# Performance work log

Measured on AMD Instinct MI355X. Metric: run time of the kernel, lower is better.

Reference implementation:

```python
import jax, jax.numpy as jnp
import numpy as np

N = 100000   # nodes
E = 800000   # undirected (unique) edges; directed count = 2*E
DV = 128; DE = 16; DH = 128; DO = 128
G = 64       # graphs in batch


def setup_inputs() -> dict:
    key = jax.random.key(0)
    ks = jax.random.split(key, 8)
    x = jax.random.normal(ks[0], (N, DV), jnp.float32)
    edge_index = jax.random.randint(ks[1], (2, 2 * E), 0, N, dtype=jnp.int32)
    edge_attr = jax.random.normal(ks[2], (E, DE), jnp.float32)
    batch = jnp.sort(jax.random.randint(ks[3], (N,), 0, G, dtype=jnp.int32))
    s = lambda k, shp, fan: jax.random.normal(k, shp, jnp.float32) / np.sqrt(fan)
    W_gcn = s(ks[4], (DV, DH), DV); b_gcn = jnp.zeros((DH,), jnp.float32)
    W_le = s(ks[5], (DE, DH), DE); b_le = jnp.zeros((DH,), jnp.float32)
    W_lin = s(ks[6], (2 * DH, DH), 2 * DH); b_lin = jnp.zeros((DH,), jnp.float32)
    W_out = s(ks[7], (DH, DO), DH); b_out = jnp.zeros((DO,), jnp.float32)
    return dict(x=x, edge_index=edge_index, edge_attr=edge_attr, batch=batch,
                W_gcn=W_gcn, b_gcn=b_gcn, W_le=W_le, b_le=b_le,
                W_lin=W_lin, b_lin=b_lin, W_out=W_out, b_out=b_out)


def reference(x, edge_index, edge_attr, batch,
              W_gcn, b_gcn, W_le, b_le, W_lin, b_lin, W_out, b_out):
    n = x.shape[0]
    loop = jnp.arange(n, dtype=edge_index.dtype)
    src = jnp.concatenate([edge_index[0], loop])  # [2E+N] with self loops
    dst = jnp.concatenate([edge_index[1], loop])

    # ---- GCNConv: symmetric norm, self-loops, lin then aggregate, + bias ----
    xw = x @ W_gcn                                      # [N, DH]
    ones_e = jnp.ones(src.shape[0], jnp.float32)
    deg = jax.ops.segment_sum(ones_e, dst, num_segments=n)  # >=1 via self loops
    dinv = jax.lax.rsqrt(deg)
    norm = dinv[src] * dinv[dst]                        # [2E+N]
    h = jax.ops.segment_sum(norm[:, None] * xw[src], dst, num_segments=n) + b_gcn
    h = jax.nn.relu(h)

    # ---- EdgeGCN: duplicate edge_attr per direction, self-loop attr = ones ----
    ea2 = jnp.repeat(edge_attr, 2, axis=0)              # [2E, DE] interleaved
    ea_full = jnp.concatenate([ea2, jnp.ones((n, edge_attr.shape[1]), jnp.float32)])
    edge_feat = ea_full @ W_le + b_le                   # [2E+N, DH]
    x_j = h[src]                                        # gather source node feats
    msg = jnp.concatenate([x_j, edge_feat], axis=-1) @ W_lin + b_lin
    h2 = jax.ops.segment_sum(msg, dst, num_segments=n)  # aggr='add'
    h2 = jax.nn.relu(h2)

    # ---- global mean pool + final linear ----
    cnt = jax.ops.segment_sum(jnp.ones(n, jnp.float32), batch, num_segments=G)
    pooled = jax.ops.segment_sum(h2, batch, num_segments=G) / jnp.maximum(cnt, 1.0)[:, None]
    return pooled @ W_out + b_out                       # [G, DO]
```

## Files before the change

### kernel.cpp

```cpp
#include <hip/hip_runtime.h>
#include <hip/hip_bf16.h>
#include <cstddef>

typedef unsigned int  u32;
typedef unsigned short u16;
typedef __attribute__((ext_vector_type(8))) short short8;
typedef __attribute__((ext_vector_type(4))) float f32x4;
typedef __attribute__((ext_vector_type(2))) float f32x2;

#define DV 128
#define DH 128
#define DE 16
#define DO 128

__device__ inline float bf_lo(u32 u){ return __uint_as_float(u << 16); }
__device__ inline float bf_hi(u32 u){ return __uint_as_float(u & 0xFFFF0000u); }
__device__ inline u32 fpack2(float a, float b){
  u32 ua = __float_as_uint(a), ub = __float_as_uint(b);
  ua += 0x7FFFu + ((ua >> 16) & 1u);
  ub += 0x7FFFu + ((ub >> 16) & 1u);
  return (ua >> 16) | (ub & 0xFFFF0000u);
}
__device__ inline u16 f2bf(float a){
  u32 ua = __float_as_uint(a); ua += 0x7FFFu + ((ua >> 16) & 1u); return (u16)(ua >> 16);
}

__device__ inline void acc_fp8(u32 s, float& a0, float& a1, float& a2, float& a3){
  f32x2 lo = __builtin_amdgcn_cvt_pk_f32_fp8((int)s, false);
  f32x2 hi = __builtin_amdgcn_cvt_pk_f32_fp8((int)s, true);
  a0 += lo.x; a1 += lo.y; a2 += hi.x; a3 += hi.y;
}
__device__ inline u32 pack_fp8(float a0, float a1, float a2, float a3){
  int o = __builtin_amdgcn_cvt_pk_fp8_f32(a0, a1, 0, false);
  o = __builtin_amdgcn_cvt_pk_fp8_f32(a2, a3, o, true);
  return (u32)o;
}

__global__ void k_init(int* cnt, float* poolp, int2* ce,
                       u32* xws_zrow, u32* h_zrow,
                       int n, int pn, int cefill, int nmark){
  int v = blockIdx.x * blockDim.x + threadIdx.x;
  if (v < n) cnt[v] = 0;
  if (v < pn) poolp[v] = 0.f;
  if (v < cefill) ce[v] = make_int2(nmark, 0);
  if (v < 32){ xws_zrow[v] = 0u; h_zrow[v] = 0u; }
}

__global__ void k_count(const int* dst, const float* edge_attr, int* cnt, int* rank,
                        u32* ea_pack, int e2){
  int j = blockIdx.x * blockDim.x + threadIdx.x;
  if (j < e2){
    rank[j] = atomicAdd(&cnt[dst[j]], 1);
    float4 f0 = *(const float4*)(edge_attr + (size_t)j * 8);
    float4 f1 = *(const float4*)(edge_attr + (size_t)j * 8 + 4);
    uint4 o;
    o.x = fpack2(f0.x, f0.y); o.y = fpack2(f0.z, f0.w);
    o.z = fpack2(f1.x, f1.y); o.w = fpack2(f1.z, f1.w);
    *(uint4*)(ea_pack + (size_t)j * 4) = o;
  }
}

__global__ __launch_bounds__(256) void k_scan1(const int* cnt, int* partial, int* bsums, int n){
  __shared__ int lds[256];
  int t = threadIdx.x;
  int base = blockIdx.x * 1024 + t * 4;
  int v0=0,v1=0,v2=0,v3=0;
  if (base + 3 < n){ int4 q = *(const int4*)(cnt + base); v0=q.x; v1=q.y; v2=q.z; v3=q.w; }
  else {
    if (base + 0 < n) v0 = cnt[base];
    if (base + 1 < n) v1 = cnt[base+1];
    if (base + 2 < n) v2 = cnt[base+2];
  }
  v0 = (v0 + 7) & ~7; v1 = (v1 + 7) & ~7; v2 = (v2 + 7) & ~7; v3 = (v3 + 7) & ~7;
  v1 += v0; v2 += v1; v3 += v2;
  lds[t] = v3; __syncthreads();
  for (int off = 1; off < 256; off <<= 1){
    int x = (t >= off) ? lds[t - off] : 0;
    __syncthreads();
    lds[t] += x;
    __syncthreads();
  }
  int add = (t > 0) ? lds[t - 1] : 0;
  if (base + 3 < n){
    int4 q; q.x = v0+add; q.y = v1+add; q.z = v2+add; q.w = v3+add;
    *(int4*)(partial + base) = q;
  } else {
    if (base + 0 < n) partial[base]   = v0 + add;
    if (base + 1 < n) partial[base+1] = v1 + add;
    if (base + 2 < n) partial[base+2] = v2 + add;
  }
  if (t == 255) bsums[blockIdx.x] = lds[255];
}

__global__ __launch_bounds__(256) void k_scan3w(const int* partial, const int* bsums, int nb,
                                                int* row_ptr, const int* cnt,
                                                float* dinv, float* degf,
                                                const int* batch, int* startg, int n, int g, int NB,
                                                const float* W_lin, const float* b_lin,
                                                const float* W_le, const float* b_le, float* Wfull){
  int bid = blockIdx.x;
  int t = threadIdx.x;
  if (bid >= NB){
    int r = (bid - NB) * 2 + (t >> 7), c = t & 127;
    if (r < DH){
      Wfull[r * DH + c] = W_lin[r * DH + c];
    } else if (r < DH + DE){
      int i = r - DH;
      float acc = 0.f;
      #pragma unroll 8
      for (int k = 0; k < DH; k += 4){
        float4 wl = *(const float4*)(W_le + i * DH + k);
        acc += wl.x * W_lin[(size_t)(DH + k    ) * DH + c];
        acc += wl.y * W_lin[(size_t)(DH + k + 1) * DH + c];
        acc += wl.z * W_lin[(size_t)(DH + k + 2) * DH + c];
        acc += wl.w * W_lin[(size_t)(DH + k + 3) * DH + c];
      }
      Wfull[r * DH + c] = acc;
    } else if (r == 144){
      float acc = b_lin[c];
      #pragma unroll 8
      for (int k = 0; k < DH; k += 4){
        float4 bl = *(const float4*)(b_le + k);
        acc += bl.x * W_lin[(size_t)(DH + k    ) * DH + c];
        acc += bl.y * W_lin[(size_t)(DH + k + 1) * DH + c];
        acc += bl.z * W_lin[(size_t)(DH + k + 2) * DH + c];
        acc += bl.w * W_lin[(size_t)(DH + k + 3) * DH + c];
      }
      Wfull[r * DH + c] = acc;
    } else if (r < 160){
      Wfull[r * DH + c] = 0.f;
    }
    return;
  }
  __shared__ int lds[128];
  if (t < 128) lds[t] = (t < nb) ? bsums[t] : 0;
  __syncthreads();
  for (int off = 1; off < 128; off <<= 1){
    int x = (t >= off && t < 128) ? lds[t - off] : 0;
    __syncthreads();
    if (t < 128) lds[t] += x;
    __syncthreads();
  }
  int i = bid * 256 + t;
  if (i < n){
    int chunk = i >> 10;
    int add = (chunk > 0) ? lds[chunk - 1] : 0;
    row_ptr[i + 1] = partial[i] + add;
    if (i == 0) row_ptr[0] = 0;
    float c = (float)(cnt[i] + 1);
    dinv[i] = rsqrtf(c);
    degf[i] = c;
    int b = batch[i];
    int prev = (i == 0) ? -1 : batch[i - 1];
    for (int q = prev + 1; q <= b; ++q) startg[q] = i;
    if (i == n - 1){ for (int q = b + 1; q <= g; ++q) startg[q] = n; }
  }
}

__global__ void k_scatter(const int* src, const int* dst, const int* rank,
                          const int* row_ptr, int2* ce, int e2){
  int j = blockIdx.x * blockDim.x + threadIdx.x;
  if (j < e2){
    int d = dst[j];
    int pos = row_ptr[d] + rank[j];
    ce[pos] = make_int2(src[j] << 5, j >> 1);
  }
}

template<int K, bool RELU, bool ABF16, bool SCALE, bool OFP8, bool POOL>
__global__ __launch_bounds__(256) void k_gemm_mfma(const void* Ap, const float* W, u32* outb,
                                                   const float* scale, int M,
                                                   const int* batchp, float* poolp){
  constexpr int SA = K + 8;
  constexpr int CS = 136;
  __shared__ u16 Wt[128 * SA];
  __shared__ u16 At[64 * SA];
  int tid = threadIdx.x;
  int row0 = blockIdx.x * 64;

  {
    int c = tid & 127, half = tid >> 7;
    for (int g = half; g < K / 8; g += 2){
      int k0 = g * 8;
      float w0 = W[(size_t)(k0+0)*128 + c], w1 = W[(size_t)(k0+1)*128 + c];
      float w2 = W[(size_t)(k0+2)*128 + c], w3 = W[(size_t)(k0+3)*128 + c];
      float w4 = W[(size_t)(k0+4)*128 + c], w5 = W[(size_t)(k0+5)*128 + c];
      float w6 = W[(size_t)(k0+6)*128 + c], w7 = W[(size_t)(k0+7)*128 + c];
      uint4 pk;
      pk.x = fpack2(w0, w1); pk.y = fpack2(w2, w3);
      pk.z = fpack2(w4, w5); pk.w = fpack2(w6, w7);
      *(uint4*)&Wt[c * SA + k0] = pk;
    }
  }
  constexpr int CH = K / 8;
  for (int idx = tid; idx < 64 * CH; idx += 256){
    int r = idx / CH, ch = idx - r * CH;
    int gr = row0 + r; if (gr > M - 1) gr = M - 1;
    uint4 pk;
    if (ABF16){
      pk = *(const uint4*)((const u16*)Ap + (size_t)gr * K + ch * 8);
    } else {
      const float* A = (const float*)Ap + (size_t)gr * K + ch * 8;
      float4 q0 = *(const float4*)A;
      float4 q1 = *(const float4*)(A + 4);
      pk.x = fpack2(q0.x, q0.y); pk.y = fpack2(q0.z, q0.w);
      pk.z = fpack2(q1.x, q1.y); pk.w = fpack2(q1.z, q1.w);
    }
    *(uint4*)&At[r * SA + ch * 8] = pk;
  }
  __syncthreads();

  int l = tid & 63, w = tid >> 6;
  int m = l & 15, quad = l >> 4;
  f32x4 acc[8];
  #pragma unroll
  for (int ct = 0; ct < 8; ++ct) acc[ct] = (f32x4){0.f, 0.f, 0.f, 0.f};
  #pragma unroll
  for (int ks = 0; ks < K; ks += 32){
    short8 av = *(const short8*)&At[(w * 16 + m) * SA + ks + quad * 8];
    #pragma unroll
    for (int ct = 0; ct < 8; ++ct){
      short8 bv = *(const short8*)&Wt[(ct * 16 + m) * SA + ks + quad * 8];
      acc[ct] = __builtin_amdgcn_mfma_f32_16x16x32_bf16(av, bv, acc[ct], 0, 0, 0);
    }
  }
  __syncthreads();

  if (POOL){
    float* ps = (float*)At;
    int rbase = w * 16 + quad * 4;
    int g0 = batchp[row0];
    int glast = batchp[(row0 + 63 < M) ? (row0 + 63) : (M - 1)];
    if (g0 == glast){
      #pragma unroll
      for (int ct = 0; ct < 8; ++ct){
        float s = 0.f;
        #pragma unroll
        for (int r = 0; r < 4; ++r){
          float vv = fmaxf(acc[ct][r], 0.f);
          if (row0 + rbase + r < M) s += vv;
        }
        s += __shfl_xor(s, 16);
        s += __shfl_xor(s, 32);
        if (quad == 0) ps[w * 128 + ct * 16 + m] = s;
      }
      __syncthreads();
      if (tid < 128){
        float t = ps[tid] + ps[128 + tid] + ps[256 + tid] + ps[384 + tid];
        atomicAdd(&poolp[g0 * DO + tid], t);
      }
    } else {
      #pragma unroll
      for (int ct = 0; ct < 8; ++ct){
        #pragma unroll
        for (int r = 0; r < 4; ++r){
          int row = row0 + rbase + r;
          if (row < M){
            float vv = fmaxf(acc[ct][r], 0.f);
            atomicAdd(&poolp[batchp[row] * DO + ct * 16 + m], vv);
          }
        }
      }
    }
    return;
  }

  u16* Ct = At;
  float sc[4];
  if (SCALE){
    #pragma unroll
    for (int r = 0; r < 4; ++r){
      int gr = row0 + w * 16 + quad * 4 + r;
      sc[r] = scale[gr < M ? gr : (M - 1)];
    }
  }
  #pragma unroll
  for (int ct = 0; ct < 8; ++ct){
    #pragma unroll
    for (int r = 0; r < 4; ++r){
      float vv = acc[ct][r];
      if (SCALE) vv *= sc[r];
      if (RELU)  vv = fmaxf(vv, 0.f);
      Ct[(w * 16 + quad * 4 + r) * CS + ct * 16 + m] = f2bf(vv);
    }
  }
  __syncthreads();
  if (OFP8){
    for (int idx = tid; idx < 64 * 16; idx += 256){
      int r = idx >> 4, c8 = idx & 15;
      int gr = row0 + r;
      if (gr < M){
        uint4 qv = *(const uint4*)&Ct[r * CS + c8 * 8];
        uint2 ov;
        ov.x = (u32)__builtin_amdgcn_cvt_pk_fp8_f32(bf_lo(qv.y), bf_hi(qv.y),
               __builtin_amdgcn_cvt_pk_fp8_f32(bf_lo(qv.x), bf_hi(qv.x), 0, false), true);
        ov.y = (u32)__builtin_amdgcn_cvt_pk_fp8_f32(bf_lo(qv.w), bf_hi(qv.w),
               __builtin_amdgcn_cvt_pk_fp8_f32(bf_lo(qv.z), bf_hi(qv.z), 0, false), true);
        *(uint2*)(outb + (size_t)gr * 32 + c8 * 2) = ov;
      }
    }
  } else {
    for (int idx = tid; idx < 64 * 16; idx += 256){
      int r = idx >> 4, ch = idx & 15;
      int gr = row0 + r;
      if (gr < M){
        uint4 q = *(const uint4*)&Ct[r * CS + ch * 8];
        *(uint4*)(outb + (size_t)gr * 64 + ch * 4) = q;
      }
    }
  }
}

__global__ __launch_bounds__(256) void k_phase1(const u32* xws8, const int* row_ptr, const int2* ce,
                                                const float* dinv, const float* b_gcn, u32* h8, int n){
  int lane = threadIdx.x & 63;
  int ln = lane & 31;
  int v = blockIdx.x * 8 + ((threadIdx.x >> 6) << 1) + (lane >> 5);
  if (v >= n) return;
  u32 sp = xws8[(size_t)v * 32 + ln];
  float a0 = 0.f, a1 = 0.f, a2 = 0.f, a3 = 0.f;
  acc_fp8(sp, a0, a1, a2, a3);
  int e0 = row_ptr[v], e1 = row_ptr[v + 1];
  int i = e0;
  u32 q0=0,q1=0,q2=0,q3=0,q4=0,q5=0,q6=0,q7=0;
  if (i < e1){
    const int4* cp = (const int4*)(ce + i);
    int4 A = cp[0], B = cp[1], C = cp[2], D = cp[3];
    q0 = xws8[A.x + ln]; q1 = xws8[A.z + ln];
    q2 = xws8[B.x + ln]; q3 = xws8[B.z + ln];
    q4 = xws8[C.x + ln]; q5 = xws8[C.z + ln];
    q6 = xws8[D.x + ln]; q7 = xws8[D.z + ln];
  }
  for (; i + 8 < e1; i += 8){
    const int4* cp2 = (const int4*)(ce + i + 8);
    int4 A = cp2[0], B = cp2[1], C = cp2[2], D = cp2[3];
    u32 p0 = xws8[A.x + ln], p1 = xws8[A.z + ln];
    u32 p2 = xws8[B.x + ln], p3 = xws8[B.z + ln];
    u32 p4 = xws8[C.x + ln], p5 = xws8[C.z + ln];
    u32 p6 = xws8[D.x + ln], p7 = xws8[D.z + ln];
    acc_fp8(q0, a0, a1, a2, a3); acc_fp8(q1, a0, a1, a2, a3);
    acc_fp8(q2, a0, a1, a2, a3); acc_fp8(q3, a0, a1, a2, a3);
    acc_fp8(q4, a0, a1, a2, a3); acc_fp8(q5, a0, a1, a2, a3);
    acc_fp8(q6, a0, a1, a2, a3); acc_fp8(q7, a0, a1, a2, a3);
    q0=p0; q1=p1; q2=p2; q3=p3; q4=p4; q5=p5; q6=p6; q7=p7;
  }
  if (i < e1){
    acc_fp8(q0, a0, a1, a2, a3); acc_fp8(q1, a0, a1, a2, a3);
    acc_fp8(q2, a0, a1, a2, a3); acc_fp8(q3, a0, a1, a2, a3);
    acc_fp8(q4, a0, a1, a2, a3); acc_fp8(q5, a0, a1, a2, a3);
    acc_fp8(q6, a0, a1, a2, a3); acc_fp8(q7, a0, a1, a2, a3);
  }
  float dv = dinv[v];
  float4 bg = *(const float4*)(b_gcn + ln * 4);
  a0 = fmaxf(fmaf(dv, a0, bg.x), 0.f);
  a1 = fmaxf(fmaf(dv, a1, bg.y), 0.f);
  a2 = fmaxf(fmaf(dv, a2, bg.z), 0.f);
  a3 = fmaxf(fmaf(dv, a3, bg.w), 0.f);
  h8[(size_t)v * 32 + ln] = pack_fp8(a0, a1, a2, a3);
}

__global__ __launch_bounds__(256) void k_phase2(const u32* h8, const int* row_ptr, const int2* ce,
                                                const u16* ea_bf, const float* degf,
                                                u16* A2b, int n){
  int lane = threadIdx.x & 63;
  int ln = lane & 31;
  int half = lane >> 5;
  int v = blockIdx.x * 8 + ((threadIdx.x >> 6) << 1) + half;
  if (v >= n) return;
  u32 sp = h8[(size_t)v * 32 + ln];
  float a0 = 0.f, a1 = 0.f, a2 = 0.f, a3 = 0.f;
  acc_fp8(sp, a0, a1, a2, a3);
  float es = 0.f;
  int ch = ln & 15, grp = ln >> 4;
  int nmark = n << 5;
  int e0 = row_ptr[v], e1 = row_ptr[v + 1];
  int i = e0;
  u32 q0=0,q1=0,q2=0,q3=0,q4=0,q5=0,q6=0,q7=0;
  int4 A = {0,0,0,0}, B = {0,0,0,0}, C = {0,0,0,0}, D = {0,0,0,0};
  if (i < e1){
    const int4* cp = (const int4*)(ce + i);
    A = cp[0]; B = cp[1]; C = cp[2]; D = cp[3];
    q0 = h8[A.x + ln]; q1 = h8[A.z + ln];
    q2 = h8[B.x + ln]; q3 = h8[B.z + ln];
    q4 = h8[C.x + ln]; q5 = h8[C.z + ln];
    q6 = h8[D.x + ln]; q7 = h8[D.z + ln];
  }
  for (; i + 8 < e1; i += 8){
    const int4* cp2 = (const int4*)(ce + i + 8);
    int4 A2 = cp2[0], B2 = cp2[1], C2 = cp2[2], D2 = cp2[3];
    int s0x = grp ? C.x : A.x, s0e = grp ? C.y : A.y;
    int s1x = grp ? C.z : A.z, s1e = grp ? C.w : A.w;
    int s2x = grp ? D.x : B.x, s2e = grp ? D.y : B.y;
    int s3x = grp ? D.z : B.z, s3e = grp ? D.w : B.w;
    float v0 = bf_lo((u32)ea_bf[(size_t)s0e * 16 + ch]);
    float v1 = bf_lo((u32)ea_bf[(size_t)s1e * 16 + ch]);
    float v2 = bf_lo((u32)ea_bf[(size_t)s2e * 16 + ch]);
    float v3 = bf_lo((u32)ea_bf[(size_t)s3e * 16 + ch]);
    u32 p0 = h8[A2.x + ln], p1 = h8[A2.z + ln];
    u32 p2 = h8[B2.x + ln], p3 = h8[B2.z + ln];
    u32 p4 = h8[C2.x + ln], p5 = h8[C2.z + ln];
    u32 p6 = h8[D2.x + ln], p7 = h8[D2.z + ln];
    acc_fp8(q0, a0, a1, a2, a3); acc_fp8(q1, a0, a1, a2, a3);
    acc_fp8(q2, a0, a1, a2, a3); acc_fp8(q3, a0, a1, a2, a3);
    acc_fp8(q4, a0, a1, a2, a3); acc_fp8(q5, a0, a1, a2, a3);
    acc_fp8(q6, a0, a1, a2, a3); acc_fp8(q7, a0, a1, a2, a3);
    es = fmaf((s0x != nmark) ? 1.f : 0.f, v0, es);
    es = fmaf((s1x != nmark) ? 1.f : 0.f, v1, es);
    es = fmaf((s2x != nmark) ? 1.f : 0.f, v2, es);
    es = fmaf((s3x != nmark) ? 1.f : 0.f, v3, es);
    q0=p0; q1=p1; q2=p2; q3=p3; q4=p4; q5=p5; q6=p6; q7=p7;
    A=A2; B=B2; C=C2; D=D2;
  }
  if (i < e1){
    int s0x = grp ? C.x : A.x, s0e = grp ? C.y : A.y;
    int s1x = grp ? C.z : A.z, s1e = grp ? C.w : A.w;
    int s2x = grp ? D.x : B.x, s2e = grp ? D.y : B.y;
    int s3x = grp ? D.z : B.z, s3e = grp ? D.w : B.w;
    float v0 = bf_lo((u32)ea_bf[(size_t)s0e * 16 + ch]);
    float v1 = bf_lo((u32)ea_bf[(size_t)s1e * 16 + ch]);
    float v2 = bf_lo((u32)ea_bf[(size_t)s2e * 16 + ch]);
    float v3 = bf_lo((u32)ea_bf[(size_t)s3e * 16 + ch]);
    acc_fp8(q0, a0, a1, a2, a3); acc_fp8(q1, a0, a1, a2, a3);
    acc_fp8(q2, a0, a1, a2, a3); acc_fp8(q3, a0, a1, a2, a3);
    acc_fp8(q4, a0, a1, a2, a3); acc_fp8(q5, a0, a1, a2, a3);
    acc_fp8(q6, a0, a1, a2, a3); acc_fp8(q7, a0, a1, a2, a3);
    es = fmaf((s0x != nmark) ? 1.f : 0.f, v0, es);
    es = fmaf((s1x != nmark) ? 1.f : 0.f, v1, es);
    es = fmaf((s2x != nmark) ? 1.f : 0.f, v2, es);
    es = fmaf((s3x != nmark) ? 1.f : 0.f, v3, es);
  }
  es += __shfl_xor(es, 16);
  float c0v = __shfl(es, half * 32 + (ln & 7) * 2);
  float c1v = __shfl(es, half * 32 + (ln & 7) * 2 + 1);
  u32* rowp = (u32*)(A2b + (size_t)v * 160);
  uint2 o; o.x = fpack2(a0, a1); o.y = fpack2(a2, a3);
  *(uint2*)(rowp + ln * 2) = o;
  if (ln < 8){
    rowp[64 + ln] = fpack2(c0v + 1.0f, c1v + 1.0f);
  } else if (ln < 16){
    rowp[64 + ln] = (ln == 8) ? (u32)f2bf(degf[v]) : 0u;
  }
}

__global__ __launch_bounds__(128) void k_poolb_final(const float* poolp, const int* start,
                                                     const float* W_out, const float* b_out,
                                                     float* out){
  __shared__ float pl[DH];
  int g = blockIdx.x, c = threadIdx.x;
  int cntg = start[g + 1] - start[g]; if (cntg < 1) cntg = 1;
  pl[c] = poolp[g * DO + c] / (float)cntg;
  __syncthreads();
  float acc = b_out[c];
  for (int k = 0; k < DH; ++k) acc += pl[k] * W_out[k * DO + c];
  out[g * DO + c] = acc;
}

extern "C" void kernel_launch(void* const* d_in, const int* in_sizes, int n_in,
                              void* d_out, int out_size, void* d_ws, size_t ws_size,
                              hipStream_t stream){
  const float* x         = (const float*)d_in[0];
  const int*   edge_index= (const int*)  d_in[1];
  const float* edge_attr = (const float*)d_in[2];
  const int*   batch     = (const int*)  d_in[3];
  const float* W_gcn     = (const float*)d_in[4];
  const float* b_gcn     = (const float*)d_in[5];
  const float* W_le      = (const float*)d_in[6];
  const float* b_le      = (const float*)d_in[7];
  const float* W_lin     = (const float*)d_in[8];
  const float* b_lin     = (const float*)d_in[9];
  const float* W_out     = (const float*)d_in[10];
  const float* b_out     = (const float*)d_in[11];
  float* out = (float*)d_out;

  const int n  = in_sizes[0] / DV;
  const int e2 = in_sizes[1] / 2;
  const int g  = out_size / DO;
  const int* srcp = edge_index;
  const int* dstp = edge_index + e2;
  const int e2pad = e2 + 7 * n + 8;

  char* ws = (char*)d_ws;
  size_t off = 0;
  auto alloc = [&](size_t bytes) -> char* {
    char* p = ws + off; off = (off + bytes + 255) & ~(size_t)255; return p;
  };

  int*   cnt     = (int*)  alloc((size_t)n * 4);
  int*   row_ptr = (int*)  alloc((size_t)(n + 1) * 4);
  int*   rank    = (int*)  alloc((size_t)e2 * 4);
  int*   partial = (int*)  alloc((size_t)n * 4);
  int*   bsums   = (int*)  alloc(512);
  float* dinv    = (float*)alloc((size_t)n * 4);
  float* degf    = (float*)alloc((size_t)n * 4);
  int*   startg  = (int*)  alloc((size_t)(g + 1) * 4);
  float* poolp   = (float*)alloc((size_t)g * DO * 4);
  float* Wfull   = (float*)alloc(160 * DH * 4);
  u32*   h8      = (u32*)  alloc((size_t)(n + 1) * 128);
  int2*  ce      = (int2*) alloc((size_t)e2pad * 8);
  u32*   ea_bf   = (u32*)  alloc((size_t)e2 * 16);
  size_t szXW = (size_t)(n + 1) * 128, szA2 = (size_t)n * 160 * 2;
  char* regionA = alloc(szA2 > szXW ? szA2 : szXW);
  u32* xws8 = (u32*)regionA;
  u16* A2b  = (u16*)regionA;

  const int nb1024 = (n + 1023) / 1024;
  const int NB = (n + 255) / 256;

  k_init   <<<(e2pad + 255) / 256, 256, 0, stream>>>(cnt, poolp, ce,
                                                     xws8 + (size_t)n * 32, h8 + (size_t)n * 32,
                                                     n, g * DO, e2pad, n << 5);
  k_count  <<<(e2 + 255) / 256, 256, 0, stream>>>(dstp, edge_attr, cnt, rank, ea_bf, e2);
  k_scan1  <<<nb1024, 256, 0, stream>>>(cnt, partial, bsums, n);
  k_scan3w <<<NB + 80, 256, 0, stream>>>(partial, bsums, nb1024, row_ptr, cnt, dinv, degf,
                                         batch, startg, n, g, NB,
                                         W_lin, b_lin, W_le, b_le, Wfull);
  k_scatter<<<(e2 + 255) / 256, 256, 0, stream>>>(srcp, dstp, rank, row_ptr, ce, e2);

  k_gemm_mfma<DV, false, false, true, true, false>
      <<<(n + 63) / 64, 256, 0, stream>>>(x, W_gcn, xws8, dinv, n, nullptr, nullptr);
  k_phase1 <<<(n + 7) / 8, 256, 0, stream>>>(xws8, row_ptr, ce, dinv, b_gcn, h8, n);
  k_phase2 <<<(n + 7) / 8, 256, 0, stream>>>(h8, row_ptr, ce,
                                             (const u16*)ea_bf, degf, A2b, n);
  k_gemm_mfma<160, true, true, false, false, true>
      <<<(n + 63) / 64, 256, 0, stream>>>(A2b, Wfull, (u32*)nullptr, (const float*)nullptr,
                                          n, batch, poolp);
  k_poolb_final<<<g, 128, 0, stream>>>(poolp, startg, W_out, b_out, out);
}
```

Before: 421.9 us.

## Merge edge scatter with first GEMM in one launch; move ce padding fill into count

```diff
diff --git a/kernel.cpp b/kernel.cpp
--- a/kernel.cpp
+++ b/kernel.cpp
@@ -36,19 +36,17 @@
   return (u32)o;
 }
 
-__global__ void k_init(int* cnt, float* poolp, int2* ce,
-                       u32* xws_zrow, u32* h_zrow,
-                       int n, int pn, int cefill, int nmark){
+__global__ void k_init(int* cnt, float* poolp, u32* xws_zrow, u32* h_zrow, int n, int pn){
   int v = blockIdx.x * blockDim.x + threadIdx.x;
   if (v < n) cnt[v] = 0;
   if (v < pn) poolp[v] = 0.f;
-  if (v < cefill) ce[v] = make_int2(nmark, 0);
   if (v < 32){ xws_zrow[v] = 0u; h_zrow[v] = 0u; }
 }
 
 __global__ void k_count(const int* dst, const float* edge_attr, int* cnt, int* rank,
-                        u32* ea_pack, int e2){
+                        u32* ea_pack, int2* ce, int e2, int cefill, int nmark){
   int j = blockIdx.x * blockDim.x + threadIdx.x;
+  int tot = gridDim.x * blockDim.x;
   if (j < e2){
     rank[j] = atomicAdd(&cnt[dst[j]], 1);
     float4 f0 = *(const float4*)(edge_attr + (size_t)j * 8);
@@ -58,6 +56,8 @@
     o.z = fpack2(f1.x, f1.y); o.w = fpack2(f1.z, f1.w);
     *(uint4*)(ea_pack + (size_t)j * 4) = o;
   }
+  int2 pd = make_int2(nmark, 0);
+  for (int i = j; i < cefill; i += tot) ce[i] = pd;
 }
 
 __global__ __launch_bounds__(256) void k_scan1(const int* cnt, int* partial, int* bsums, int n){
@@ -157,13 +157,94 @@
   }
 }
 
-__global__ void k_scatter(const int* src, const int* dst, const int* rank,
-                          const int* row_ptr, int2* ce, int e2){
-  int j = blockIdx.x * blockDim.x + threadIdx.x;
-  if (j < e2){
-    int d = dst[j];
-    int pos = row_ptr[d] + rank[j];
-    ce[pos] = make_int2(src[j] << 5, j >> 1);
+__global__ __launch_bounds__(256) void k_scatter_g1(const int* src, const int* dst, const int* rank,
+                                                    const int* row_ptr, int2* ce, int e2, int SB,
+                                                    const float* x, const float* W,
+                                                    const float* dinv, u32* xws8, int M){
+  __shared__ u16 lds_u[64 * 136];
+  int bid = blockIdx.x;
+  int tid = threadIdx.x;
+  if (bid < SB){
+    int j = bid * 256 + tid;
+    if (j < e2){
+      int d = dst[j];
+      int pos = row_ptr[d] + rank[j];
+      ce[pos] = make_int2(src[j] << 5, j >> 1);
+    }
+    return;
+  }
+  int row0 = (bid - SB) * 64;
+  u16* Wt = lds_u;
+  u16* At = lds_u + 128 * 40;
+  int l = tid & 63, w = tid >> 6;
+  int m = l & 15, quad = l >> 4;
+  f32x4 acc[8];
+  #pragma unroll
+  for (int ct = 0; ct < 8; ++ct) acc[ct] = (f32x4){0.f, 0.f, 0.f, 0.f};
+  for (int ks = 0; ks < DV; ks += 32){
+    __syncthreads();
+    {
+      int c = tid & 127, hh = tid >> 7;
+      #pragma unroll
+      for (int g2 = 0; g2 < 2; ++g2){
+        int k0 = hh * 16 + g2 * 8;
+        const float* Wp = W + (size_t)(ks + k0) * 128 + c;
+        float w0 = Wp[0*128], w1 = Wp[1*128], w2 = Wp[2*128], w3 = Wp[3*128];
+        float w4 = Wp[4*128], w5 = Wp[5*128], w6 = Wp[6*128], w7 = Wp[7*128];
+        uint4 pk;
+        pk.x = fpack2(w0, w1); pk.y = fpack2(w2, w3);
+        pk.z = fpack2(w4, w5); pk.w = fpack2(w6, w7);
+        *(uint4*)&Wt[c * 40 + k0] = pk;
+      }
+    }
+    {
+      int r = tid >> 2, ch = tid & 3;
+      int gr = row0 + r; if (gr > M - 1) gr = M - 1;
+      const float* A = x + (size_t)gr * DV + ks + ch * 8;
+      float4 q0 = *(const float4*)A;
+      float4 q1 = *(const float4*)(A + 4);
+      uint4 pk;
+      pk.x = fpack2(q0.x, q0.y); pk.y = fpack2(q0.z, q0.w);
+      pk.z = fpack2(q1.x, q1.y); pk.w = fpack2(q1.z, q1.w);
+      *(uint4*)&At[r * 40 + ch * 8] = pk;
+    }
+    __syncthreads();
+    short8 av = *(const short8*)&At[(w * 16 + m) * 40 + quad * 8];
+    #pragma unroll
+    for (int ct = 0; ct < 8; ++ct){
+      short8 bv = *(const short8*)&Wt[(ct * 16 + m) * 40 + quad * 8];
+      acc[ct] = __builtin_amdgcn_mfma_f32_16x16x32_bf16(av, bv, acc[ct], 0, 0, 0);
+    }
+  }
+  __syncthreads();
+  u16* Ct = lds_u;
+  float sc[4];
+  #pragma unroll
+  for (int r = 0; r < 4; ++r){
+    int gr = row0 + w * 16 + quad * 4 + r;
+    sc[r] = dinv[gr < M ? gr : (M - 1)];
+  }
+  #pragma unroll
+  for (int ct = 0; ct < 8; ++ct){
+    #pragma unroll
+    for (int r = 0; r < 4; ++r){
+      float vv = acc[ct][r] * sc[r];
+      Ct[(w * 16 + quad * 4 + r) * 136 + ct * 16 + m] = f2bf(vv);
+    }
+  }
+  __syncthreads();
+  for (int idx = tid; idx < 64 * 16; idx += 256){
+    int r = idx >> 4, c8 = idx & 15;
+    int gr = row0 + r;
+    if (gr < M){
+      uint4 qv = *(const uint4*)&Ct[r * 136 + c8 * 8];
+      uint2 ov;
+      ov.x = (u32)__builtin_amdgcn_cvt_pk_fp8_f32(bf_lo(qv.y), bf_hi(qv.y),
+             __builtin_amdgcn_cvt_pk_fp8_f32(bf_lo(qv.x), bf_hi(qv.x), 0, false), true);
+      ov.y = (u32)__builtin_amdgcn_cvt_pk_fp8_f32(bf_lo(qv.w), bf_hi(qv.w),
+             __builtin_amdgcn_cvt_pk_fp8_f32(bf_lo(qv.z), bf_hi(qv.z), 0, false), true);
+      *(uint2*)(xws8 + (size_t)gr * 32 + c8 * 2) = ov;
+    }
   }
 }
 
@@ -505,22 +586,23 @@
 
   const int nb1024 = (n + 1023) / 1024;
   const int NB = (n + 255) / 256;
-
-  k_init   <<<(e2pad + 255) / 256, 256, 0, stream>>>(cnt, poolp, ce,
-                                                     xws8 + (size_t)n * 32, h8 + (size_t)n * 32,
-                                                     n, g * DO, e2pad, n << 5);
-  k_count  <<<(e2 + 255) / 256, 256, 0, stream>>>(dstp, edge_attr, cnt, rank, ea_bf, e2);
-  k_scan1  <<<nb1024, 256, 0, stream>>>(cnt, partial, bsums, n);
-  k_scan3w <<<NB + 80, 256, 0, stream>>>(partial, bsums, nb1024, row_ptr, cnt, dinv, degf,
-                                         batch, startg, n, g, NB,
-                                         W_lin, b_lin, W_le, b_le, Wfull);
-  k_scatter<<<(e2 + 255) / 256, 256, 0, stream>>>(srcp, dstp, rank, row_ptr, ce, e2);
-
-  k_gemm_mfma<DV, false, false, true, true, false>
-      <<<(n + 63) / 64, 256, 0, stream>>>(x, W_gcn, xws8, dinv, n, nullptr, nullptr);
-  k_phase1 <<<(n + 7) / 8, 256, 0, stream>>>(xws8, row_ptr, ce, dinv, b_gcn, h8, n);
-  k_phase2 <<<(n + 7) / 8, 256, 0, stream>>>(h8, row_ptr, ce,
-                                             (const u16*)ea_bf, degf, A2b, n);
+  const int SB = (e2 + 255) / 256;
+  const int GB = (n + 63) / 64;
+
+  k_init      <<<(n + 255) / 256, 256, 0, stream>>>(cnt, poolp,
+                                                    xws8 + (size_t)n * 32, h8 + (size_t)n * 32,
+                                                    n, g * DO);
+  k_count     <<<SB, 256, 0, stream>>>(dstp, edge_attr, cnt, rank, ea_bf, ce,
+                                       e2, e2pad, n << 5);
+  k_scan1     <<<nb1024, 256, 0, stream>>>(cnt, partial, bsums, n);
+  k_scan3w    <<<NB + 80, 256, 0, stream>>>(partial, bsums, nb1024, row_ptr, cnt, dinv, degf,
+                                            batch, startg, n, g, NB,
+                                            W_lin, b_lin, W_le, b_le, Wfull);
+  k_scatter_g1<<<SB + GB, 256, 0, stream>>>(srcp, dstp, rank, row_ptr, ce, e2, SB,
+                                            x, W_gcn, dinv, xws8, n);
+  k_phase1    <<<(n + 7) / 8, 256, 0, stream>>>(xws8, row_ptr, ce, dinv, b_gcn, h8, n);
+  k_phase2    <<<(n + 7) / 8, 256, 0, stream>>>(h8, row_ptr, ce,
+                                                (const u16*)ea_bf, degf, A2b, n);
   k_gemm_mfma<160, true, true, false, false, true>
       <<<(n + 63) / 64, 256, 0, stream>>>(A2b, Wfull, (u32*)nullptr, (const float*)nullptr,
                                           n, batch, poolp);
```

Result: faster. 405.3 us (-3.9%).
